# Kernel optimization log

Measured on AMD Instinct MI355X. Metric: run time of the kernel, lower is better.

The kernel has to match this reference:

```python
import jax, jax.numpy as jnp
import numpy as np

N_USERS = 100000
N_ITEMS = 400000
N_NODES = N_USERS + N_ITEMS
NNZ = 4000000
EMB = 64
N_LAYERS = 3


def setup_inputs() -> dict:
    key = jax.random.key(0)
    k1, k2, k3, k4, k5 = jax.random.split(key, 5)
    user_emb = 0.1 * jax.random.normal(k1, (N_USERS, EMB), dtype=jnp.float32)
    item_emb = 0.1 * jax.random.normal(k2, (N_ITEMS, EMB), dtype=jnp.float32)
    adj_rows = jax.random.randint(k3, (NNZ,), 0, N_NODES, dtype=jnp.int32)
    adj_cols = jax.random.randint(k4, (NNZ,), 0, N_NODES, dtype=jnp.int32)
    # positive normalized-Laplacian-like values
    adj_vals = jax.random.uniform(k5, (NNZ,), dtype=jnp.float32) * 0.1
    return {"user_emb": user_emb, "item_emb": item_emb,
            "adj_rows": adj_rows, "adj_cols": adj_cols, "adj_vals": adj_vals}


def _spmm(rows, cols, vals, x):
    # y[r] += vals * x[cols]  (COO SpMM with skinny dense features)
    msgs = vals[:, None] * x[cols]            # [nnz, EMB]
    return jax.ops.segment_sum(msgs, rows, num_segments=N_NODES)


def reference(user_emb, item_emb, adj_rows, adj_cols, adj_vals):
    e = jnp.concatenate([user_emb, item_emb], axis=0)  # [N, EMB]
    acc = e
    cur = e
    for _ in range(N_LAYERS):
        cur = _spmm(adj_rows, adj_cols, adj_vals, cur)
        acc = acc + cur
    final = acc / jnp.asarray(N_LAYERS + 1, dtype=e.dtype)  # mean over stacked layers
    return final[:N_USERS], final[N_USERS:]
```

## Files before the change

kernel.cpp:

```cpp
#include <hip/hip_runtime.h>

#define N_USERS  100000
#define N_ITEMS  400000
#define N_NODES  500000
#define NNZ_CNT  4000000
#define EMB      64

#define BBITS    11
#define BROWS    (1 << BBITS)
#define NB       ((N_NODES + BROWS - 1) >> BBITS)
#define COLBITS  19
#define COLMASK  ((1 << COLBITS) - 1)
#define CAP      17408

#define VQ_SCALE 81910.0f
#define VQ_DEQ   (1.0f / 81910.0f)

#define PART_CHUNK 4096
#define NPARTBLK ((NNZ_CNT + PART_CHUNK - 1) / PART_CHUNK)
#define TOBFBLK  ((N_NODES * 8 + 511) / 512)

typedef unsigned uint4v __attribute__((ext_vector_type(4)));
typedef float    float4v __attribute__((ext_vector_type(4)));

__device__ __forceinline__ unsigned bf16rne(float f) {
    unsigned b = __float_as_uint(f);
    return (b + 0x7FFFu + ((b >> 16) & 1u)) >> 16;
}
__device__ __forceinline__ unsigned pack2(float lo, float hi) {
    return bf16rne(lo) | (bf16rne(hi) << 16);
}
__device__ __forceinline__ float blo(unsigned u) { return __uint_as_float(u << 16); }
__device__ __forceinline__ float bhi(unsigned u) { return __uint_as_float(u & 0xFFFF0000u); }

__device__ __forceinline__ unsigned fp8e(float y) {
    float c = fminf(fmaxf(y, -440.f), 440.f);
    unsigned b = __float_as_uint(c);
    unsigned s = (b >> 24) & 0x80u;
    int e = (int)((b >> 23) & 0xFF) - 120;
    if (e <= 0) return s;
    unsigned m = b & 0x7FFFFFu;
    unsigned r = (m + 0x7FFFFu + ((m >> 20) & 1u)) >> 20;
    return s | ((unsigned)(e << 3) + r);
}
__device__ __forceinline__ float fp8d(unsigned u) {
    return __uint_as_float(((u & 0x80u) << 24) | ((u & 0x7Fu) << 20));
}

__global__ __launch_bounds__(512)
void lgcn_binit(int* __restrict__ bcur) {
    int t = threadIdx.x;
    if (t < NB) bcur[t] = t * CAP;
}

__global__ __launch_bounds__(512)
void lgcn_part_tobf(const int* __restrict__ rows, const int* __restrict__ cols,
                    const float* __restrict__ vals, int* __restrict__ bcur,
                    int2* __restrict__ part,
                    const float4* __restrict__ user, const float4* __restrict__ item,
                    uint4v* __restrict__ ebf) {
    __shared__ int h[NB];
    __shared__ int scanl[NB + 1];
    __shared__ int gb[NB];
    __shared__ int cur[NB];
    __shared__ int   stage_lo[PART_CHUNK];
    __shared__ float stage_v[PART_CHUNK];

    int t = threadIdx.x;

    if (blockIdx.x >= NPARTBLK) {
        int i = (blockIdx.x - NPARTBLK) * 512 + t;
        if (i >= N_NODES * 8) return;
        int f4 = i * 2;
        const int NU4 = N_USERS * 16;
        float4 a, b;
        if (f4 < NU4) { a = user[f4]; b = user[f4 + 1]; }
        else          { a = item[f4 - NU4]; b = item[f4 + 1 - NU4]; }
        uint4v o;
        o.x = pack2(a.x, a.y); o.y = pack2(a.z, a.w);
        o.z = pack2(b.x, b.y); o.w = pack2(b.z, b.w);
        ebf[i] = o;
        return;
    }

    int e0 = blockIdx.x * PART_CHUNK;
    int n  = NNZ_CNT - e0; if (n > PART_CHUNK) n = PART_CHUNK;

    if (t < NB) h[t] = 0;
    __syncthreads();

    int pk[8]; float pv[8]; int pb[8];
#pragma unroll
    for (int k = 0; k < 8; ++k) {
        int i = k * 512 + t;
        pb[k] = -1;
        if (i < n) {
            int e = e0 + i;
            int r = rows[e];
            int b = r >> BBITS;
            pb[k] = b;
            pk[k] = ((r & (BROWS - 1)) << COLBITS) | cols[e];
            pv[k] = vals[e];
            atomicAdd(&h[b], 1);
        }
    }
    __syncthreads();
    if (t == 0) {
        int run = 0;
        for (int b = 0; b < NB; ++b) { scanl[b] = run; run += h[b]; }
        scanl[NB] = run;
    }
    __syncthreads();
    if (t < NB) { gb[t] = atomicAdd(&bcur[t], h[t]); cur[t] = scanl[t]; }
    __syncthreads();
#pragma unroll
    for (int k = 0; k < 8; ++k) {
        if (pb[k] >= 0) {
            int lp = atomicAdd(&cur[pb[k]], 1);
            stage_lo[lp] = pk[k];
            stage_v[lp]  = pv[k];
        }
    }
    __syncthreads();
    for (int s = t; s < n; s += 512) {
        int lo = 0, hi = NB;
        while (hi - lo > 1) {
            int mid = (lo + hi) >> 1;
            if (scanl[mid] <= s) lo = mid; else hi = mid;
        }
        int pos = gb[lo] + (s - scanl[lo]);
        if (pos < (lo + 1) * CAP)
            part[pos] = make_int2(stage_lo[s], __float_as_int(stage_v[s]));
    }
}

__global__ __launch_bounds__(1024)
void lgcn_rscanb(const int2* __restrict__ part, const int* __restrict__ bcur,
                 int* __restrict__ rs, int* __restrict__ re,
                 unsigned* __restrict__ cv) {
    __shared__ int h[BROWS];
    __shared__ int tsum[1024];
    int b = blockIdx.x, t = threadIdx.x;
    int s = b * CAP;
    int e = bcur[b]; if (e > s + CAP) e = s + CAP;
    h[t] = 0; h[t + 1024] = 0;
    __syncthreads();
    for (int j = s + t; j < e; j += 1024)
        atomicAdd(&h[((unsigned)part[j].x) >> COLBITS], 1);
    __syncthreads();
    int v0 = h[2 * t], v1 = h[2 * t + 1];
    int sum = v0 + v1;
    tsum[t] = sum;
    __syncthreads();
    for (int off = 1; off < 1024; off <<= 1) {
        int x = (t >= off) ? tsum[t - off] : 0;
        __syncthreads();
        tsum[t] += x;
        __syncthreads();
    }
    int base = s + tsum[t] - sum;
    int r0 = (b << BBITS) + 2 * t;
    if (r0 < N_NODES)     { rs[r0]     = base;      re[r0]     = base + v0; }
    if (r0 + 1 < N_NODES) { rs[r0 + 1] = base + v0; re[r0 + 1] = base + v0 + v1; }
    __syncthreads();
    h[2 * t] = base; h[2 * t + 1] = base + v0;
    __syncthreads();
    for (int j = s + t; j < e; j += 1024) {
        int2 p = part[j];
        int rlo = ((unsigned)p.x) >> COLBITS;
        int pos = atomicAdd(&h[rlo], 1);
        float val = __int_as_float(p.y);
        unsigned vq = (unsigned)__float2int_rn(val * VQ_SCALE);
        if (vq > 8191u) vq = 8191u;
        cv[pos] = (vq << COLBITS) | ((unsigned)p.x & COLMASK);
    }
}

template <int MODE>
__global__ __launch_bounds__(256, 4)
void lgcn_gatherb(const int* __restrict__ rs_, const int* __restrict__ re_,
                  const unsigned* __restrict__ cv,
                  const uint4v* __restrict__ xsrc,
                  uint4v* __restrict__ xdst,
                  uint2* __restrict__ x2q,
                  const uint2* __restrict__ xq,
                  const uint4v* __restrict__ ebf,
                  const uint4v* __restrict__ x1,
                  float4v* __restrict__ out) {
    int tid = blockIdx.x * blockDim.x + threadIdx.x;
    if (tid >= N_NODES * 8) return;
    int row = tid >> 3;
    int c   = tid & 7;
    int s = rs_[row];
    int e = re_[row];
    float a0 = 0.f, a1 = 0.f, a2 = 0.f, a3 = 0.f;
    float a4 = 0.f, a5 = 0.f, a6 = 0.f, a7 = 0.f;
    int j = s;
    if (MODE < 2) {
        for (; j + 4 <= e; j += 4) {
            unsigned w0 = __builtin_nontemporal_load(&cv[j]);
            unsigned w1 = __builtin_nontemporal_load(&cv[j + 1]);
            unsigned w2 = __builtin_nontemporal_load(&cv[j + 2]);
            unsigned w3 = __builtin_nontemporal_load(&cv[j + 3]);
            uint4v u0 = xsrc[(size_t)(w0 & COLMASK) * 8 + c];
            uint4v u1 = xsrc[(size_t)(w1 & COLMASK) * 8 + c];
            uint4v u2 = xsrc[(size_t)(w2 & COLMASK) * 8 + c];
            uint4v u3 = xsrc[(size_t)(w3 & COLMASK) * 8 + c];
            float v0 = (float)(w0 >> COLBITS) * VQ_DEQ;
            float v1 = (float)(w1 >> COLBITS) * VQ_DEQ;
            float v2 = (float)(w2 >> COLBITS) * VQ_DEQ;
            float v3 = (float)(w3 >> COLBITS) * VQ_DEQ;
            a0 += v0 * blo(u0.x); a1 += v0 * bhi(u0.x);
            a2 += v0 * blo(u0.y); a3 += v0 * bhi(u0.y);
            a4 += v0 * blo(u0.z); a5 += v0 * bhi(u0.z);
            a6 += v0 * blo(u0.w); a7 += v0 * bhi(u0.w);
            a0 += v1 * blo(u1.x); a1 += v1 * bhi(u1.x);
            a2 += v1 * blo(u1.y); a3 += v1 * bhi(u1.y);
            a4 += v1 * blo(u1.z); a5 += v1 * bhi(u1.z);
            a6 += v1 * blo(u1.w); a7 += v1 * bhi(u1.w);
            a0 += v2 * blo(u2.x); a1 += v2 * bhi(u2.x);
            a2 += v2 * blo(u2.y); a3 += v2 * bhi(u2.y);
            a4 += v2 * blo(u2.z); a5 += v2 * bhi(u2.z);
            a6 += v2 * blo(u2.w); a7 += v2 * bhi(u2.w);
            a0 += v3 * blo(u3.x); a1 += v3 * bhi(u3.x);
            a2 += v3 * blo(u3.y); a3 += v3 * bhi(u3.y);
            a4 += v3 * blo(u3.z); a5 += v3 * bhi(u3.z);
            a6 += v3 * blo(u3.w); a7 += v3 * bhi(u3.w);
        }
        for (; j < e; ++j) {
            unsigned w = __builtin_nontemporal_load(&cv[j]);
            uint4v u = xsrc[(size_t)(w & COLMASK) * 8 + c];
            float v = (float)(w >> COLBITS) * VQ_DEQ;
            a0 += v * blo(u.x); a1 += v * bhi(u.x);
            a2 += v * blo(u.y); a3 += v * bhi(u.y);
            a4 += v * blo(u.z); a5 += v * bhi(u.z);
            a6 += v * blo(u.w); a7 += v * bhi(u.w);
        }
    } else {
        for (; j + 4 <= e; j += 4) {
            unsigned w0 = __builtin_nontemporal_load(&cv[j]);
            unsigned w1 = __builtin_nontemporal_load(&cv[j + 1]);
            unsigned w2 = __builtin_nontemporal_load(&cv[j + 2]);
            unsigned w3 = __builtin_nontemporal_load(&cv[j + 3]);
            uint2 q0 = xq[(size_t)(w0 & COLMASK) * 8 + c];
            uint2 q1 = xq[(size_t)(w1 & COLMASK) * 8 + c];
            uint2 q2 = xq[(size_t)(w2 & COLMASK) * 8 + c];
            uint2 q3 = xq[(size_t)(w3 & COLMASK) * 8 + c];
            float k0 = (float)(w0 >> COLBITS) * (VQ_DEQ * 0x1p+108f);
            float k1 = (float)(w1 >> COLBITS) * (VQ_DEQ * 0x1p+108f);
            float k2 = (float)(w2 >> COLBITS) * (VQ_DEQ * 0x1p+108f);
            float k3 = (float)(w3 >> COLBITS) * (VQ_DEQ * 0x1p+108f);
            a0 += k0 * fp8d(q0.x);       a1 += k0 * fp8d(q0.x >> 8);
            a2 += k0 * fp8d(q0.x >> 16); a3 += k0 * fp8d(q0.x >> 24);
            a4 += k0 * fp8d(q0.y);       a5 += k0 * fp8d(q0.y >> 8);
            a6 += k0 * fp8d(q0.y >> 16); a7 += k0 * fp8d(q0.y >> 24);
            a0 += k1 * fp8d(q1.x);       a1 += k1 * fp8d(q1.x >> 8);
            a2 += k1 * fp8d(q1.x >> 16); a3 += k1 * fp8d(q1.x >> 24);
            a4 += k1 * fp8d(q1.y);       a5 += k1 * fp8d(q1.y >> 8);
            a6 += k1 * fp8d(q1.y >> 16); a7 += k1 * fp8d(q1.y >> 24);
            a0 += k2 * fp8d(q2.x);       a1 += k2 * fp8d(q2.x >> 8);
            a2 += k2 * fp8d(q2.x >> 16); a3 += k2 * fp8d(q2.x >> 24);
            a4 += k2 * fp8d(q2.y);       a5 += k2 * fp8d(q2.y >> 8);
            a6 += k2 * fp8d(q2.y >> 16); a7 += k2 * fp8d(q2.y >> 24);
            a0 += k3 * fp8d(q3.x);       a1 += k3 * fp8d(q3.x >> 8);
            a2 += k3 * fp8d(q3.x >> 16); a3 += k3 * fp8d(q3.x >> 24);
            a4 += k3 * fp8d(q3.y);       a5 += k3 * fp8d(q3.y >> 8);
            a6 += k3 * fp8d(q3.y >> 16); a7 += k3 * fp8d(q3.y >> 24);
        }
        for (; j < e; ++j) {
            unsigned w = __builtin_nontemporal_load(&cv[j]);
            uint2 q = xq[(size_t)(w & COLMASK) * 8 + c];
            float k = (float)(w >> COLBITS) * (VQ_DEQ * 0x1p+108f);
            a0 += k * fp8d(q.x);       a1 += k * fp8d(q.x >> 8);
            a2 += k * fp8d(q.x >> 16); a3 += k * fp8d(q.x >> 24);
            a4 += k * fp8d(q.y);       a5 += k * fp8d(q.y >> 8);
            a6 += k * fp8d(q.y >> 16); a7 += k * fp8d(q.y >> 24);
        }
    }
    if (MODE < 2) {
        uint4v o;
        o.x = pack2(a0, a1); o.y = pack2(a2, a3);
        o.z = pack2(a4, a5); o.w = pack2(a6, a7);
        xdst[tid] = o;
        if (MODE == 1) {
            unsigned qa = fp8e(a0 * 4096.f) | (fp8e(a1 * 4096.f) << 8) |
                          (fp8e(a2 * 4096.f) << 16) | (fp8e(a3 * 4096.f) << 24);
            unsigned qb = fp8e(a4 * 4096.f) | (fp8e(a5 * 4096.f) << 8) |
                          (fp8e(a6 * 4096.f) << 16) | (fp8e(a7 * 4096.f) << 24);
            x2q[tid] = make_uint2(qa, qb);
        }
    } else {
        uint4v e8 = __builtin_nontemporal_load(&ebf[tid]);
        uint4v u1 = __builtin_nontemporal_load(&x1[tid]);
        uint4v u2 = xsrc[tid];
        float4v o0, o1;
        o0.x = 0.25f * (blo(e8.x) + blo(u1.x) + blo(u2.x) + a0);
        o0.y = 0.25f * (bhi(e8.x) + bhi(u1.x) + bhi(u2.x) + a1);
        o0.z = 0.25f * (blo(e8.y) + blo(u1.y) + blo(u2.y) + a2);
        o0.w = 0.25f * (bhi(e8.y) + bhi(u1.y) + bhi(u2.y) + a3);
        o1.x = 0.25f * (blo(e8.z) + blo(u1.z) + blo(u2.z) + a4);
        o1.y = 0.25f * (bhi(e8.z) + bhi(u1.z) + bhi(u2.z) + a5);
        o1.z = 0.25f * (blo(e8.w) + blo(u1.w) + blo(u2.w) + a6);
        o1.w = 0.25f * (bhi(e8.w) + bhi(u1.w) + bhi(u2.w) + a7);
        __builtin_nontemporal_store(o0, &out[(size_t)tid * 2]);
        __builtin_nontemporal_store(o1, &out[(size_t)tid * 2 + 1]);
    }
}

extern "C" void kernel_launch(void* const* d_in, const int* in_sizes, int n_in,
                              void* d_out, int out_size, void* d_ws, size_t ws_size,
                              hipStream_t stream) {
    const float* user = (const float*)d_in[0];
    const float* item = (const float*)d_in[1];
    const int*   rows = (const int*)d_in[2];
    const int*   cols = (const int*)d_in[3];
    const float* vals = (const float*)d_in[4];
    float* out = (float*)d_out;

    char* ws = (char*)d_ws;
    unsigned* cv   = (unsigned*)(ws);
    int2*   part   = (int2*)(ws + 17100800);
    uint4v* ebf    = (uint4v*)(ws + 51220480);
    uint4v* x1     = (uint4v*)(ws + 115220480);
    uint4v* x2     = (uint4v*)(ws + 179220480);
    uint2*  x2q    = (uint2*)(ws + 243220480);
    int*    rs     = (int*)(ws + 275220480);
    int*    re     = (int*)(ws + 277220544);
    int*    bcur   = (int*)(ws + 279220608);

    lgcn_binit<<<1, 512, 0, stream>>>(bcur);
    lgcn_part_tobf<<<NPARTBLK + TOBFBLK, 512, 0, stream>>>(
        rows, cols, vals, bcur, part, (const float4*)user, (const float4*)item, ebf);
    lgcn_rscanb<<<NB, 1024, 0, stream>>>(part, bcur, rs, re, cv);

    const int gblocks = (N_NODES * 8 + 255) / 256;
    lgcn_gatherb<0><<<gblocks, 256, 0, stream>>>(
        rs, re, cv, ebf, x1, nullptr, nullptr, nullptr, nullptr, nullptr);
    lgcn_gatherb<1><<<gblocks, 256, 0, stream>>>(
        rs, re, cv, x1, x2, x2q, nullptr, nullptr, nullptr, nullptr);
    lgcn_gatherb<2><<<gblocks, 256, 0, stream>>>(
        rs, re, cv, x2, nullptr, nullptr, x2q, ebf, x1, (float4v*)out);
}
```

Baseline: 457.3 us.

## Drop fp8 layer-3 gather path, use bf16 throughout; store bucket ids in partition

Removes the fp8 quantized copy of the second-layer embeddings, so the third gather reads bf16 rows like the other layers and mode 1 no longer writes the extra fp8 array. The partition kernel now records each staged entry's bucket id in shared memory instead of binary-searching the scan for every output element. Layer outputs are written with nontemporal stores. The last gather moves twice as many bytes per neighbour row but does less decode work and gains accuracy.

```diff
diff --git a/kernel.cpp b/kernel.cpp
--- a/kernel.cpp
+++ b/kernel.cpp
@@ -32,20 +32,6 @@
 }
 __device__ __forceinline__ float blo(unsigned u) { return __uint_as_float(u << 16); }
 __device__ __forceinline__ float bhi(unsigned u) { return __uint_as_float(u & 0xFFFF0000u); }
-
-__device__ __forceinline__ unsigned fp8e(float y) {
-    float c = fminf(fmaxf(y, -440.f), 440.f);
-    unsigned b = __float_as_uint(c);
-    unsigned s = (b >> 24) & 0x80u;
-    int e = (int)((b >> 23) & 0xFF) - 120;
-    if (e <= 0) return s;
-    unsigned m = b & 0x7FFFFFu;
-    unsigned r = (m + 0x7FFFFu + ((m >> 20) & 1u)) >> 20;
-    return s | ((unsigned)(e << 3) + r);
-}
-__device__ __forceinline__ float fp8d(unsigned u) {
-    return __uint_as_float(((u & 0x80u) << 24) | ((u & 0x7Fu) << 20));
-}
 
 __global__ __launch_bounds__(512)
 void lgcn_binit(int* __restrict__ bcur) {
@@ -60,11 +46,12 @@
                     const float4* __restrict__ user, const float4* __restrict__ item,
                     uint4v* __restrict__ ebf) {
     __shared__ int h[NB];
-    __shared__ int scanl[NB + 1];
+    __shared__ int scanl[NB];
     __shared__ int gb[NB];
     __shared__ int cur[NB];
     __shared__ int   stage_lo[PART_CHUNK];
     __shared__ float stage_v[PART_CHUNK];
+    __shared__ unsigned char stage_b[PART_CHUNK];
 
     int t = threadIdx.x;
 
@@ -108,7 +95,6 @@
     if (t == 0) {
         int run = 0;
         for (int b = 0; b < NB; ++b) { scanl[b] = run; run += h[b]; }
-        scanl[NB] = run;
     }
     __syncthreads();
     if (t < NB) { gb[t] = atomicAdd(&bcur[t], h[t]); cur[t] = scanl[t]; }
@@ -119,17 +105,14 @@
             int lp = atomicAdd(&cur[pb[k]], 1);
             stage_lo[lp] = pk[k];
             stage_v[lp]  = pv[k];
+            stage_b[lp]  = (unsigned char)pb[k];
         }
     }
     __syncthreads();
     for (int s = t; s < n; s += 512) {
-        int lo = 0, hi = NB;
-        while (hi - lo > 1) {
-            int mid = (lo + hi) >> 1;
-            if (scanl[mid] <= s) lo = mid; else hi = mid;
-        }
-        int pos = gb[lo] + (s - scanl[lo]);
-        if (pos < (lo + 1) * CAP)
+        int b = stage_b[s];
+        int pos = gb[b] + (s - scanl[b]);
+        if (pos < (b + 1) * CAP)
             part[pos] = make_int2(stage_lo[s], __float_as_int(stage_v[s]));
     }
 }
@@ -182,8 +165,6 @@
                   const unsigned* __restrict__ cv,
                   const uint4v* __restrict__ xsrc,
                   uint4v* __restrict__ xdst,
-                  uint2* __restrict__ x2q,
-                  const uint2* __restrict__ xq,
                   const uint4v* __restrict__ ebf,
                   const uint4v* __restrict__ x1,
                   float4v* __restrict__ out) {
@@ -196,99 +177,50 @@
     float a0 = 0.f, a1 = 0.f, a2 = 0.f, a3 = 0.f;
     float a4 = 0.f, a5 = 0.f, a6 = 0.f, a7 = 0.f;
     int j = s;
-    if (MODE < 2) {
-        for (; j + 4 <= e; j += 4) {
-            unsigned w0 = __builtin_nontemporal_load(&cv[j]);
-            unsigned w1 = __builtin_nontemporal_load(&cv[j + 1]);
-            unsigned w2 = __builtin_nontemporal_load(&cv[j + 2]);
-            unsigned w3 = __builtin_nontemporal_load(&cv[j + 3]);
-            uint4v u0 = xsrc[(size_t)(w0 & COLMASK) * 8 + c];
-            uint4v u1 = xsrc[(size_t)(w1 & COLMASK) * 8 + c];
-            uint4v u2 = xsrc[(size_t)(w2 & COLMASK) * 8 + c];
-            uint4v u3 = xsrc[(size_t)(w3 & COLMASK) * 8 + c];
-            float v0 = (float)(w0 >> COLBITS) * VQ_DEQ;
-            float v1 = (float)(w1 >> COLBITS) * VQ_DEQ;
-            float v2 = (float)(w2 >> COLBITS) * VQ_DEQ;
-            float v3 = (float)(w3 >> COLBITS) * VQ_DEQ;
-            a0 += v0 * blo(u0.x); a1 += v0 * bhi(u0.x);
-            a2 += v0 * blo(u0.y); a3 += v0 * bhi(u0.y);
-            a4 += v0 * blo(u0.z); a5 += v0 * bhi(u0.z);
-            a6 += v0 * blo(u0.w); a7 += v0 * bhi(u0.w);
-            a0 += v1 * blo(u1.x); a1 += v1 * bhi(u1.x);
-            a2 += v1 * blo(u1.y); a3 += v1 * bhi(u1.y);
-            a4 += v1 * blo(u1.z); a5 += v1 * bhi(u1.z);
-            a6 += v1 * blo(u1.w); a7 += v1 * bhi(u1.w);
-            a0 += v2 * blo(u2.x); a1 += v2 * bhi(u2.x);
-            a2 += v2 * blo(u2.y); a3 += v2 * bhi(u2.y);
-            a4 += v2 * blo(u2.z); a5 += v2 * bhi(u2.z);
-            a6 += v2 * blo(u2.w); a7 += v2 * bhi(u2.w);
-            a0 += v3 * blo(u3.x); a1 += v3 * bhi(u3.x);
-            a2 += v3 * blo(u3.y); a3 += v3 * bhi(u3.y);
-            a4 += v3 * blo(u3.z); a5 += v3 * bhi(u3.z);
-            a6 += v3 * blo(u3.w); a7 += v3 * bhi(u3.w);
-        }
-        for (; j < e; ++j) {
-            unsigned w = __builtin_nontemporal_load(&cv[j]);
-            uint4v u = xsrc[(size_t)(w & COLMASK) * 8 + c];
-            float v = (float)(w >> COLBITS) * VQ_DEQ;
-            a0 += v * blo(u.x); a1 += v * bhi(u.x);
-            a2 += v * blo(u.y); a3 += v * bhi(u.y);
-            a4 += v * blo(u.z); a5 += v * bhi(u.z);
-            a6 += v * blo(u.w); a7 += v * bhi(u.w);
-        }
-    } else {
-        for (; j + 4 <= e; j += 4) {
-            unsigned w0 = __builtin_nontemporal_load(&cv[j]);
-            unsigned w1 = __builtin_nontemporal_load(&cv[j + 1]);
-            unsigned w2 = __builtin_nontemporal_load(&cv[j + 2]);
-            unsigned w3 = __builtin_nontemporal_load(&cv[j + 3]);
-            uint2 q0 = xq[(size_t)(w0 & COLMASK) * 8 + c];
-            uint2 q1 = xq[(size_t)(w1 & COLMASK) * 8 + c];
-            uint2 q2 = xq[(size_t)(w2 & COLMASK) * 8 + c];
-            uint2 q3 = xq[(size_t)(w3 & COLMASK) * 8 + c];
-            float k0 = (float)(w0 >> COLBITS) * (VQ_DEQ * 0x1p+108f);
-            float k1 = (float)(w1 >> COLBITS) * (VQ_DEQ * 0x1p+108f);
-            float k2 = (float)(w2 >> COLBITS) * (VQ_DEQ * 0x1p+108f);
-            float k3 = (float)(w3 >> COLBITS) * (VQ_DEQ * 0x1p+108f);
-            a0 += k0 * fp8d(q0.x);       a1 += k0 * fp8d(q0.x >> 8);
-            a2 += k0 * fp8d(q0.x >> 16); a3 += k0 * fp8d(q0.x >> 24);
-            a4 += k0 * fp8d(q0.y);       a5 += k0 * fp8d(q0.y >> 8);
-            a6 += k0 * fp8d(q0.y >> 16); a7 += k0 * fp8d(q0.y >> 24);
-            a0 += k1 * fp8d(q1.x);       a1 += k1 * fp8d(q1.x >> 8);
-            a2 += k1 * fp8d(q1.x >> 16); a3 += k1 * fp8d(q1.x >> 24);
-            a4 += k1 * fp8d(q1.y);       a5 += k1 * fp8d(q1.y >> 8);
-            a6 += k1 * fp8d(q1.y >> 16); a7 += k1 * fp8d(q1.y >> 24);
-            a0 += k2 * fp8d(q2.x);       a1 += k2 * fp8d(q2.x >> 8);
-            a2 += k2 * fp8d(q2.x >> 16); a3 += k2 * fp8d(q2.x >> 24);
-            a4 += k2 * fp8d(q2.y);       a5 += k2 * fp8d(q2.y >> 8);
-            a6 += k2 * fp8d(q2.y >> 16); a7 += k2 * fp8d(q2.y >> 24);
-            a0 += k3 * fp8d(q3.x);       a1 += k3 * fp8d(q3.x >> 8);
-            a2 += k3 * fp8d(q3.x >> 16); a3 += k3 * fp8d(q3.x >> 24);
-            a4 += k3 * fp8d(q3.y);       a5 += k3 * fp8d(q3.y >> 8);
-            a6 += k3 * fp8d(q3.y >> 16); a7 += k3 * fp8d(q3.y >> 24);
-        }
-        for (; j < e; ++j) {
-            unsigned w = __builtin_nontemporal_load(&cv[j]);
-            uint2 q = xq[(size_t)(w & COLMASK) * 8 + c];
-            float k = (float)(w >> COLBITS) * (VQ_DEQ * 0x1p+108f);
-            a0 += k * fp8d(q.x);       a1 += k * fp8d(q.x >> 8);
-            a2 += k * fp8d(q.x >> 16); a3 += k * fp8d(q.x >> 24);
-            a4 += k * fp8d(q.y);       a5 += k * fp8d(q.y >> 8);
-            a6 += k * fp8d(q.y >> 16); a7 += k * fp8d(q.y >> 24);
-        }
+    for (; j + 4 <= e; j += 4) {
+        unsigned w0 = __builtin_nontemporal_load(&cv[j]);
+        unsigned w1 = __builtin_nontemporal_load(&cv[j + 1]);
+        unsigned w2 = __builtin_nontemporal_load(&cv[j + 2]);
+        unsigned w3 = __builtin_nontemporal_load(&cv[j + 3]);
+        uint4v u0 = xsrc[(size_t)(w0 & COLMASK) * 8 + c];
+        uint4v u1 = xsrc[(size_t)(w1 & COLMASK) * 8 + c];
+        uint4v u2 = xsrc[(size_t)(w2 & COLMASK) * 8 + c];
+        uint4v u3 = xsrc[(size_t)(w3 & COLMASK) * 8 + c];
+        float v0 = (float)(w0 >> COLBITS) * VQ_DEQ;
+        float v1 = (float)(w1 >> COLBITS) * VQ_DEQ;
+        float v2 = (float)(w2 >> COLBITS) * VQ_DEQ;
+        float v3 = (float)(w3 >> COLBITS) * VQ_DEQ;
+        a0 += v0 * blo(u0.x); a1 += v0 * bhi(u0.x);
+        a2 += v0 * blo(u0.y); a3 += v0 * bhi(u0.y);
+        a4 += v0 * blo(u0.z); a5 += v0 * bhi(u0.z);
+        a6 += v0 * blo(u0.w); a7 += v0 * bhi(u0.w);
+        a0 += v1 * blo(u1.x); a1 += v1 * bhi(u1.x);
+        a2 += v1 * blo(u1.y); a3 += v1 * bhi(u1.y);
+        a4 += v1 * blo(u1.z); a5 += v1 * bhi(u1.z);
+        a6 += v1 * blo(u1.w); a7 += v1 * bhi(u1.w);
+        a0 += v2 * blo(u2.x); a1 += v2 * bhi(u2.x);
+        a2 += v2 * blo(u2.y); a3 += v2 * bhi(u2.y);
+        a4 += v2 * blo(u2.z); a5 += v2 * bhi(u2.z);
+        a6 += v2 * blo(u2.w); a7 += v2 * bhi(u2.w);
+        a0 += v3 * blo(u3.x); a1 += v3 * bhi(u3.x);
+        a2 += v3 * blo(u3.y); a3 += v3 * bhi(u3.y);
+        a4 += v3 * blo(u3.z); a5 += v3 * bhi(u3.z);
+        a6 += v3 * blo(u3.w); a7 += v3 * bhi(u3.w);
+    }
+    for (; j < e; ++j) {
+        unsigned w = __builtin_nontemporal_load(&cv[j]);
+        uint4v u = xsrc[(size_t)(w & COLMASK) * 8 + c];
+        float v = (float)(w >> COLBITS) * VQ_DEQ;
+        a0 += v * blo(u.x); a1 += v * bhi(u.x);
+        a2 += v * blo(u.y); a3 += v * bhi(u.y);
+        a4 += v * blo(u.z); a5 += v * bhi(u.z);
+        a6 += v * blo(u.w); a7 += v * bhi(u.w);
     }
     if (MODE < 2) {
         uint4v o;
         o.x = pack2(a0, a1); o.y = pack2(a2, a3);
         o.z = pack2(a4, a5); o.w = pack2(a6, a7);
-        xdst[tid] = o;
-        if (MODE == 1) {
-            unsigned qa = fp8e(a0 * 4096.f) | (fp8e(a1 * 4096.f) << 8) |
-                          (fp8e(a2 * 4096.f) << 16) | (fp8e(a3 * 4096.f) << 24);
-            unsigned qb = fp8e(a4 * 4096.f) | (fp8e(a5 * 4096.f) << 8) |
-                          (fp8e(a6 * 4096.f) << 16) | (fp8e(a7 * 4096.f) << 24);
-            x2q[tid] = make_uint2(qa, qb);
-        }
+        __builtin_nontemporal_store(o, &xdst[tid]);
     } else {
         uint4v e8 = __builtin_nontemporal_load(&ebf[tid]);
         uint4v u1 = __builtin_nontemporal_load(&x1[tid]);
@@ -323,10 +255,9 @@
     uint4v* ebf    = (uint4v*)(ws + 51220480);
     uint4v* x1     = (uint4v*)(ws + 115220480);
     uint4v* x2     = (uint4v*)(ws + 179220480);
-    uint2*  x2q    = (uint2*)(ws + 243220480);
-    int*    rs     = (int*)(ws + 275220480);
-    int*    re     = (int*)(ws + 277220544);
-    int*    bcur   = (int*)(ws + 279220608);
+    int*    rs     = (int*)(ws + 243220480);
+    int*    re     = (int*)(ws + 245220544);
+    int*    bcur   = (int*)(ws + 247220608);
 
     lgcn_binit<<<1, 512, 0, stream>>>(bcur);
     lgcn_part_tobf<<<NPARTBLK + TOBFBLK, 512, 0, stream>>>(
@@ -335,9 +266,9 @@
 
     const int gblocks = (N_NODES * 8 + 255) / 256;
     lgcn_gatherb<0><<<gblocks, 256, 0, stream>>>(
-        rs, re, cv, ebf, x1, nullptr, nullptr, nullptr, nullptr, nullptr);
+        rs, re, cv, ebf, x1, nullptr, nullptr, nullptr);
     lgcn_gatherb<1><<<gblocks, 256, 0, stream>>>(
-        rs, re, cv, x1, x2, x2q, nullptr, nullptr, nullptr, nullptr);
+        rs, re, cv, x1, x2, nullptr, nullptr, nullptr);
     lgcn_gatherb<2><<<gblocks, 256, 0, stream>>>(
-        rs, re, cv, x2, nullptr, nullptr, x2q, ebf, x1, (float4v*)out);
-}
+        rs, re, cv, x2, nullptr, ebf, x1, (float4v*)out);
+}
```

Result: no change. 449.9 us (-1.6%).
